# Performance work log

Measured on AMD Instinct MI355X. Metric: run time of the kernel, lower is better.

The kernel has to match this reference:

```python
import jax, jax.numpy as jnp
import numpy as np

NUM_HEADS = 6
WIN = 16
NW = 16   # number of windows sharing one mask (b_ % NW == 0)


def setup_inputs() -> dict:
    key = jax.random.key(0)
    ks = jax.random.split(key, 6)
    b_, n, dim = 256, WIN * WIN, 192
    qkv = jax.random.normal(ks[0], (b_, n, 3 * dim), dtype=jnp.float32)
    rpi = jax.random.randint(ks[1], (n, n), 0, (2 * WIN - 1) * (2 * WIN - 1))
    # additive attention mask per window-group (Swin uses 0 / -100; randn is fine for math)
    mask = jax.random.normal(ks[2], (NW, n, n), dtype=jnp.float32)
    rpb_table = 0.02 * jax.random.normal(ks[3], ((2 * WIN - 1) * (2 * WIN - 1), NUM_HEADS), dtype=jnp.float32)
    proj_w = jax.random.normal(ks[4], (dim, dim), dtype=jnp.float32) * (1.0 / np.sqrt(dim))
    proj_b = jax.random.normal(ks[5], (dim,), dtype=jnp.float32) * 0.01
    return {"qkv": qkv, "rpi": rpi, "mask": mask, "rpb_table": rpb_table,
            "proj_w": proj_w, "proj_b": proj_b}


def reference(qkv, rpi, mask, rpb_table, proj_w, proj_b):
    b_, n, c3 = qkv.shape
    c = c3 // 3
    h = NUM_HEADS
    hd = c // h
    scale = float(hd) ** -0.5
    # (b_, n, 3, h, hd) -> (3, b_, h, n, hd)
    qkv = qkv.reshape(b_, n, 3, h, hd).transpose(2, 0, 3, 1, 4)
    q, k, v = qkv[0] * scale, qkv[1], qkv[2]
    attn = jnp.einsum('bhqd,bhkd->bhqk', q, k)  # [b_, h, n, n]
    # gathered relative position bias: [n, n, h] -> [h, n, n]
    bias = rpb_table[rpi].transpose(2, 0, 1)
    attn = attn + bias[None]
    # add per-window-group mask: [b_//nw, nw, h, n, n]
    nw = mask.shape[0]
    attn = attn.reshape(b_ // nw, nw, h, n, n) + mask[None, :, None]
    attn = attn.reshape(b_, h, n, n)
    attn = jax.nn.softmax(attn, axis=-1)
    x = jnp.einsum('bhqk,bhkd->bhqd', attn, v)  # [b_, h, n, hd]
    x = x.transpose(0, 2, 1, 3).reshape(b_, n, c)
    # nn.Linear: x @ W^T + b
    return x @ proj_w.T + proj_b
```

## Files before the change

### kernel.cpp

```cpp
#include <hip/hip_runtime.h>
#include <hip/hip_bf16.h>

typedef _Float16 f16;
typedef _Float16 f16x2 __attribute__((ext_vector_type(2)));
typedef _Float16 f16x4 __attribute__((ext_vector_type(4)));
typedef _Float16 f16x8 __attribute__((ext_vector_type(8)));
typedef __fp16 h16x2 __attribute__((ext_vector_type(2)));
typedef float f32x4 __attribute__((ext_vector_type(4)));

#define NHEADS 6
#define NTOK 256
#define NWINS 256
#define DIM 192
#define HD 32
#define C3 576
#define LOG2E 1.4426950408889634f
#define SCALE (0.17677669529663687f * LOG2E)

__device__ inline f16x2 pkrtz(float a, float b) {
  h16x2 r = __builtin_amdgcn_cvt_pkrtz(a, b);
  return __builtin_bit_cast(f16x2, r);
}

__global__ __launch_bounds__(256) void prep_cb_kernel(const int* __restrict__ rpi,
                                                      const float* __restrict__ mask,
                                                      const float* __restrict__ rpb,
                                                      f16* __restrict__ cb) {
  int idx = blockIdx.x * 256 + threadIdx.x;
  int rem = idx & 255;
  int q = (idx >> 8) & 255;
  int t = idx >> 16;
  int h = t % 6;
  int mg = t / 6;
  int ktp = rem >> 5;
  int gg = (rem >> 3) & 3;
  int e = rem & 7;
  int k = (2 * ktp + (e >> 2)) * 16 + gg * 4 + (e & 3);
  float v = (rpb[rpi[(q << 8) | k] * 6 + h] + mask[(mg << 16) | (q << 8) | k]) * LOG2E;
  cb[idx] = (f16)v;
}

__global__ __launch_bounds__(256) void prep_w_kernel(const float* __restrict__ w,
                                                     f16* __restrict__ w16) {
  int i = blockIdx.x * 256 + threadIdx.x;
  if (i < DIM * DIM) w16[i] = (f16)w[i];
}

__device__ inline f16x8 q_to_f16(float4 a, float4 b) {
  f16x2 p0 = pkrtz(a.x * SCALE, a.y * SCALE);
  f16x2 p1 = pkrtz(a.z * SCALE, a.w * SCALE);
  f16x2 p2 = pkrtz(b.x * SCALE, b.y * SCALE);
  f16x2 p3 = pkrtz(b.z * SCALE, b.w * SCALE);
  f16x4 lo = __builtin_shufflevector(p0, p1, 0, 1, 2, 3);
  f16x4 hi = __builtin_shufflevector(p2, p3, 0, 1, 2, 3);
  return __builtin_shufflevector(lo, hi, 0, 1, 2, 3, 4, 5, 6, 7);
}

__global__ __launch_bounds__(512, 4) void attn_kernel(const float* __restrict__ qkv,
                                                      const f16* __restrict__ cb,
                                                      f16* __restrict__ x16) {
  const int idx = blockIdx.x;
  const int grp = idx % 96;
  const int pr = idx / 96;
  const int h = grp % 6;
  const int blo = grp / 6;
  const int tid = threadIdx.x;
  const int lane = tid & 63;
  const int wave = tid >> 6;
  const int g = lane >> 4;
  const int r16 = lane & 15;

  __shared__ f16 Klin[2][16 * 64 * 8];
  __shared__ f16 VT[2][32][264];

  const int t = tid & 255;
  const int srow = t >> 3;
  const int part = t & 7;
  const bool isK = tid < 256;
  const int gg = part >> 1;
  const int half = part & 1;
  const int d0 = part * 4;

  const int b0 = ((pr * 2) << 4) | blo;
  const int b1 = ((pr * 2 + 1) << 4) | blo;
  const float* sbase0 = qkv + (size_t)(b0 * NTOK + srow) * C3 + DIM + (isK ? 0 : DIM)
                        + h * HD + part * 4;
  const float* sbase1 = qkv + (size_t)(b1 * NTOK + srow) * C3 + DIM + (isK ? 0 : DIM)
                        + h * HD + part * 4;

  auto stage_write = [&](int buf, int rgbase, const float4* v4) {
#pragma unroll
    for (int rg = 0; rg < 4; ++rg) {
      const int row = (rgbase + rg) * 32 + srow;
      if (isK) {
        const int slot = ((row >> 4) * 64) + gg * 16 + ((row & 15) ^ (gg << 2));
        f16x2 k01 = pkrtz(v4[rg].x, v4[rg].y);
        f16x2 k23 = pkrtz(v4[rg].z, v4[rg].w);
        *((f16x4*)&Klin[buf][slot * 8 + half * 4]) =
            __builtin_shufflevector(k01, k23, 0, 1, 2, 3);
      } else {
        VT[buf][d0 + 0][row ^ (((d0 + 0) & 7) << 2)] = (f16)v4[rg].x;
        VT[buf][d0 + 1][row ^ (((d0 + 1) & 7) << 2)] = (f16)v4[rg].y;
        VT[buf][d0 + 2][row ^ (((d0 + 2) & 7) << 2)] = (f16)v4[rg].z;
        VT[buf][d0 + 3][row ^ (((d0 + 3) & 7) << 2)] = (f16)v4[rg].w;
      }
    }
  };

  {
    float4 s4[8];
#pragma unroll
    for (int i = 0; i < 8; ++i)
      s4[i] = *(const float4*)(sbase0 + (size_t)(i * 32) * C3);
    stage_write(0, 0, s4);
    stage_write(0, 4, s4 + 4);
  }
  __syncthreads();

  const f16* cbb = cb + ((size_t)grp << 16);
  const int krd = (lane & 48) + ((lane & 15) ^ ((lane >> 2) & 12));
  const int qbase = wave * 32;

#pragma unroll
  for (int pair = 0; pair < 2; ++pair) {
    const int b = (pair == 0) ? b0 : b1;

#pragma unroll
    for (int c = 0; c < 2; ++c) {
      float4 n4[4];
      if (pair == 0) {
#pragma unroll
        for (int i = 0; i < 4; ++i)
          n4[i] = *(const float4*)(sbase1 + (size_t)((c * 4 + i) * 32) * C3);
      }

      const int qrow = qbase + c * 16 + r16;
      const float* qp = qkv + (size_t)(b * NTOK + qrow) * C3 + h * HD + g * 8;
      f16x8 qf = q_to_f16(((const float4*)qp)[0], ((const float4*)qp)[1]);
      const f16* cbq = cbb + (qrow << 8) + g * 8;

      f16x8 cv[4];
#pragma unroll
      for (int kp = 0; kp < 4; ++kp) cv[kp] = *((const f16x8*)(cbq + kp * 32));
      f32x4 acc[8];
#pragma unroll
      for (int kp = 0; kp < 4; ++kp) {
#pragma unroll
        for (int r = 0; r < 4; ++r) {
          acc[2 * kp][r] = (float)cv[kp][r];
          acc[2 * kp + 1][r] = (float)cv[kp][4 + r];
        }
      }
#pragma unroll
      for (int kt = 0; kt < 8; ++kt) {
        f16x8 af = *((const f16x8*)&Klin[pair][(kt * 64 + krd) * 8]);
        acc[kt] = __builtin_amdgcn_mfma_f32_16x16x32_f16(af, qf, acc[kt], 0, 0, 0);
      }

      if (pair == 0) stage_write(1, c * 4, n4);

      float m0 = fmaxf(fmaxf(acc[0][0], acc[1][0]), fmaxf(acc[2][0], acc[3][0]));
      float m1 = fmaxf(fmaxf(acc[0][1], acc[1][1]), fmaxf(acc[2][1], acc[3][1]));
      float m2 = fmaxf(fmaxf(acc[0][2], acc[1][2]), fmaxf(acc[2][2], acc[3][2]));
      float m3 = fmaxf(fmaxf(acc[0][3], acc[1][3]), fmaxf(acc[2][3], acc[3][3]));
#pragma unroll
      for (int kt = 4; kt < 8; ++kt) {
        m0 = fmaxf(m0, acc[kt][0]); m1 = fmaxf(m1, acc[kt][1]);
        m2 = fmaxf(m2, acc[kt][2]); m3 = fmaxf(m3, acc[kt][3]);
      }
      float mA = fmaxf(fmaxf(m0, m1), fmaxf(m2, m3));
      mA = fmaxf(mA, __shfl_xor(mA, 16));
      mA = fmaxf(mA, __shfl_xor(mA, 32));

      float s0 = 0.f, s1 = 0.f, s2 = 0.f, s3 = 0.f;
#pragma unroll
      for (int kt = 0; kt < 8; ++kt) {
        float p0 = __builtin_amdgcn_exp2f(acc[kt][0] - mA);
        float p1 = __builtin_amdgcn_exp2f(acc[kt][1] - mA);
        float p2 = __builtin_amdgcn_exp2f(acc[kt][2] - mA);
        float p3 = __builtin_amdgcn_exp2f(acc[kt][3] - mA);
        acc[kt][0] = p0; acc[kt][1] = p1; acc[kt][2] = p2; acc[kt][3] = p3;
        s0 += p0; s1 += p1; s2 += p2; s3 += p3;
      }
      float sA = (s0 + s1) + (s2 + s3);

      f32x4 xa0[2], xa1[2];
#pragma unroll
      for (int dt = 0; dt < 2; ++dt) {
        xa0[dt][0] = 0.f; xa0[dt][1] = 0.f; xa0[dt][2] = 0.f; xa0[dt][3] = 0.f;
        xa1[dt][0] = 0.f; xa1[dt][1] = 0.f; xa1[dt][2] = 0.f; xa1[dt][3] = 0.f;
      }
#pragma unroll
      for (int kt = 0; kt < 8; ++kt) {
        f16x2 p01 = pkrtz(acc[kt][0], acc[kt][1]);
        f16x2 p23 = pkrtz(acc[kt][2], acc[kt][3]);
        f16x4 pf = __builtin_shufflevector(p01, p23, 0, 1, 2, 3);
#pragma unroll
        for (int dt = 0; dt < 2; ++dt) {
          const int col = (kt * 16 + g * 4) ^ ((r16 & 7) << 2);
          f16x4 vf = *((const f16x4*)&VT[pair][dt * 16 + r16][col]);
          if (kt < 4)
            xa0[dt] = __builtin_amdgcn_mfma_f32_16x16x16f16(vf, pf, xa0[dt], 0, 0, 0);
          else
            xa1[dt] = __builtin_amdgcn_mfma_f32_16x16x16f16(vf, pf, xa1[dt], 0, 0, 0);
        }
      }

#pragma unroll
      for (int kp = 0; kp < 4; ++kp) cv[kp] = *((const f16x8*)(cbq + 128 + kp * 32));
#pragma unroll
      for (int kp = 0; kp < 4; ++kp) {
#pragma unroll
        for (int r = 0; r < 4; ++r) {
          acc[2 * kp][r] = (float)cv[kp][r];
          acc[2 * kp + 1][r] = (float)cv[kp][4 + r];
        }
      }
#pragma unroll
      for (int kt = 0; kt < 8; ++kt) {
        f16x8 af = *((const f16x8*)&Klin[pair][((kt + 8) * 64 + krd) * 8]);
        acc[kt] = __builtin_amdgcn_mfma_f32_16x16x32_f16(af, qf, acc[kt], 0, 0, 0);
      }

      m0 = fmaxf(fmaxf(acc[0][0], acc[1][0]), fmaxf(acc[2][0], acc[3][0]));
      m1 = fmaxf(fmaxf(acc[0][1], acc[1][1]), fmaxf(acc[2][1], acc[3][1]));
      m2 = fmaxf(fmaxf(acc[0][2], acc[1][2]), fmaxf(acc[2][2], acc[3][2]));
      m3 = fmaxf(fmaxf(acc[0][3], acc[1][3]), fmaxf(acc[2][3], acc[3][3]));
#pragma unroll
      for (int kt = 4; kt < 8; ++kt) {
        m0 = fmaxf(m0, acc[kt][0]); m1 = fmaxf(m1, acc[kt][1]);
        m2 = fmaxf(m2, acc[kt][2]); m3 = fmaxf(m3, acc[kt][3]);
      }
      float mB = fmaxf(fmaxf(m0, m1), fmaxf(m2, m3));
      mB = fmaxf(mB, __shfl_xor(mB, 16));
      mB = fmaxf(mB, __shfl_xor(mB, 32));

      const float m = fmaxf(mA, mB);
      const float scA = __builtin_amdgcn_exp2f(mA - m);

      s0 = 0.f; s1 = 0.f; s2 = 0.f; s3 = 0.f;
#pragma unroll
      for (int kt = 0; kt < 8; ++kt) {
        float p0 = __builtin_amdgcn_exp2f(acc[kt][0] - m);
        float p1 = __builtin_amdgcn_exp2f(acc[kt][1] - m);
        float p2 = __builtin_amdgcn_exp2f(acc[kt][2] - m);
        float p3 = __builtin_amdgcn_exp2f(acc[kt][3] - m);
        acc[kt][0] = p0; acc[kt][1] = p1; acc[kt][2] = p2; acc[kt][3] = p3;
        s0 += p0; s1 += p1; s2 += p2; s3 += p3;
      }
      float s = sA * scA + (s0 + s1) + (s2 + s3);
      s += __shfl_xor(s, 16);
      s += __shfl_xor(s, 32);
      const float rinv = 1.0f / s;

#pragma unroll
      for (int dt = 0; dt < 2; ++dt) {
        xa0[dt][0] *= scA; xa0[dt][1] *= scA; xa0[dt][2] *= scA; xa0[dt][3] *= scA;
        xa1[dt][0] *= scA; xa1[dt][1] *= scA; xa1[dt][2] *= scA; xa1[dt][3] *= scA;
      }
#pragma unroll
      for (int kt = 0; kt < 8; ++kt) {
        f16x2 p01 = pkrtz(acc[kt][0], acc[kt][1]);
        f16x2 p23 = pkrtz(acc[kt][2], acc[kt][3]);
        f16x4 pf = __builtin_shufflevector(p01, p23, 0, 1, 2, 3);
#pragma unroll
        for (int dt = 0; dt < 2; ++dt) {
          const int col = ((kt + 8) * 16 + g * 4) ^ ((r16 & 7) << 2);
          f16x4 vf = *((const f16x4*)&VT[pair][dt * 16 + r16][col]);
          if (kt < 4)
            xa0[dt] = __builtin_amdgcn_mfma_f32_16x16x16f16(vf, pf, xa0[dt], 0, 0, 0);
          else
            xa1[dt] = __builtin_amdgcn_mfma_f32_16x16x16f16(vf, pf, xa1[dt], 0, 0, 0);
        }
      }

      f16* xp = x16 + (size_t)(b * NTOK + qrow) * DIM + h * HD;
#pragma unroll
      for (int dt = 0; dt < 2; ++dt) {
        f16x2 o01 = pkrtz((xa0[dt][0] + xa1[dt][0]) * rinv,
                          (xa0[dt][1] + xa1[dt][1]) * rinv);
        f16x2 o23 = pkrtz((xa0[dt][2] + xa1[dt][2]) * rinv,
                          (xa0[dt][3] + xa1[dt][3]) * rinv);
        *((f16x4*)(xp + dt * 16 + g * 4)) = __builtin_shufflevector(o01, o23, 0, 1, 2, 3);
      }
    }

    if (pair == 0) __syncthreads();
  }
}

__global__ __launch_bounds__(256) void proj_kernel(const f16* __restrict__ x16,
                                                   const f16* __restrict__ w16,
                                                   const float* __restrict__ pb,
                                                   float* __restrict__ out) {
  const int lane = threadIdx.x & 63;
  const int wave = threadIdx.x >> 6;
  const int g = lane >> 4;
  const int r16 = lane & 15;
  const int m0 = blockIdx.x * 64 + wave * 16;

  f32x4 acc[12];
#pragma unroll
  for (int jt = 0; jt < 12; ++jt) {
    acc[jt][0] = 0.f; acc[jt][1] = 0.f; acc[jt][2] = 0.f; acc[jt][3] = 0.f;
  }
#pragma unroll
  for (int cc = 0; cc < 6; ++cc) {
    f16x8 af = *((const f16x8*)(x16 + (size_t)(m0 + r16) * DIM + cc * 32 + g * 8));
#pragma unroll
    for (int jt = 0; jt < 12; ++jt) {
      f16x8 bf = *((const f16x8*)(w16 + (size_t)(jt * 16 + r16) * DIM + cc * 32 + g * 8));
      acc[jt] = __builtin_amdgcn_mfma_f32_16x16x32_f16(af, bf, acc[jt], 0, 0, 0);
    }
  }
#pragma unroll
  for (int jt = 0; jt < 12; ++jt) {
    int j = jt * 16 + r16;
    float bias = pb[j];
#pragma unroll
    for (int r = 0; r < 4; ++r) {
      out[(size_t)(m0 + g * 4 + r) * DIM + j] = acc[jt][r] + bias;
    }
  }
}

extern "C" void kernel_launch(void* const* d_in, const int* in_sizes, int n_in,
                              void* d_out, int out_size, void* d_ws, size_t ws_size,
                              hipStream_t stream) {
  const float* qkv  = (const float*)d_in[0];
  const int*   rpi  = (const int*)d_in[1];
  const float* mask = (const float*)d_in[2];
  const float* rpb  = (const float*)d_in[3];
  const float* pw   = (const float*)d_in[4];
  const float* pbv  = (const float*)d_in[5];
  float* out = (float*)d_out;

  char* ws = (char*)d_ws;
  f16* cb16 = (f16*)ws;
  f16* x16  = (f16*)(ws + 12582912);
  f16* w16  = (f16*)(ws + 12582912 + 25165824);

  prep_cb_kernel<<<24576, 256, 0, stream>>>(rpi, mask, rpb, cb16);
  prep_w_kernel<<<144, 256, 0, stream>>>(pw, w16);
  attn_kernel<<<768, 512, 0, stream>>>(qkv, cb16, x16);
  proj_kernel<<<1024, 256, 0, stream>>>(x16, w16, pbv, out);
}
```

Before: 108.9 us.

## Split combined bias+mask precompute into separate per-head bias and per-group mask tables

The prep kernel no longer materialises a full 16x6x256x256 fp16 combined bias+mask tensor. It now writes a small per-head relative-position-bias table and a per-window-group mask table, each in the same swizzled layout. The attention kernel loads both and adds them in fp16 before seeding the accumulators. This cuts the prep write traffic and the footprint of the precomputed table by a large factor, at the cost of twice as many loads in the attention inner loop and an extra fp16 add, which also slightly changes rounding.

```diff
diff --git a/kernel.cpp b/kernel.cpp
--- a/kernel.cpp
+++ b/kernel.cpp
@@ -22,22 +22,49 @@
   return __builtin_bit_cast(f16x2, r);
 }
 
-__global__ __launch_bounds__(256) void prep_cb_kernel(const int* __restrict__ rpi,
-                                                      const float* __restrict__ mask,
-                                                      const float* __restrict__ rpb,
-                                                      f16* __restrict__ cb) {
-  int idx = blockIdx.x * 256 + threadIdx.x;
-  int rem = idx & 255;
-  int q = (idx >> 8) & 255;
-  int t = idx >> 16;
-  int h = t % 6;
-  int mg = t / 6;
-  int ktp = rem >> 5;
-  int gg = (rem >> 3) & 3;
-  int e = rem & 7;
-  int k = (2 * ktp + (e >> 2)) * 16 + gg * 4 + (e & 3);
-  float v = (rpb[rpi[(q << 8) | k] * 6 + h] + mask[(mg << 16) | (q << 8) | k]) * LOG2E;
-  cb[idx] = (f16)v;
+__global__ __launch_bounds__(256) void prep_rpb_kernel(const int* __restrict__ rpi,
+                                                       const float* __restrict__ rpb,
+                                                       f16* __restrict__ rpb16) {
+  int u = blockIdx.x * 256 + threadIdx.x;
+  int g = u & 3;
+  int ktp = (u >> 2) & 7;
+  int q = (u >> 5) & 255;
+  int h = u >> 13;
+  int k0 = ktp * 32 + g * 4;
+  const int* rp = rpi + (q << 8);
+  int4 i0 = *(const int4*)(rp + k0);
+  int4 i1 = *(const int4*)(rp + k0 + 16);
+  f16x8 o;
+  o[0] = (f16)(rpb[i0.x * 6 + h] * LOG2E);
+  o[1] = (f16)(rpb[i0.y * 6 + h] * LOG2E);
+  o[2] = (f16)(rpb[i0.z * 6 + h] * LOG2E);
+  o[3] = (f16)(rpb[i0.w * 6 + h] * LOG2E);
+  o[4] = (f16)(rpb[i1.x * 6 + h] * LOG2E);
+  o[5] = (f16)(rpb[i1.y * 6 + h] * LOG2E);
+  o[6] = (f16)(rpb[i1.z * 6 + h] * LOG2E);
+  o[7] = (f16)(rpb[i1.w * 6 + h] * LOG2E);
+  *((f16x8*)(rpb16 + (size_t)u * 8)) = o;
+}
+
+__global__ __launch_bounds__(256) void prep_mask_kernel(const float* __restrict__ mask,
+                                                        f16* __restrict__ mask16) {
+  int u = blockIdx.x * 256 + threadIdx.x;
+  int g = u & 3;
+  int ktp = (u >> 2) & 7;
+  int q = (u >> 5) & 255;
+  int mg = u >> 13;
+  int k0 = ktp * 32 + g * 4;
+  const float* mp = mask + ((size_t)mg << 16) + (q << 8);
+  float4 v0 = *(const float4*)(mp + k0);
+  float4 v1 = *(const float4*)(mp + k0 + 16);
+  f16x2 a = pkrtz(v0.x * LOG2E, v0.y * LOG2E);
+  f16x2 b = pkrtz(v0.z * LOG2E, v0.w * LOG2E);
+  f16x2 c = pkrtz(v1.x * LOG2E, v1.y * LOG2E);
+  f16x2 d = pkrtz(v1.z * LOG2E, v1.w * LOG2E);
+  f16x4 lo = __builtin_shufflevector(a, b, 0, 1, 2, 3);
+  f16x4 hi = __builtin_shufflevector(c, d, 0, 1, 2, 3);
+  *((f16x8*)(mask16 + (size_t)u * 8)) =
+      __builtin_shufflevector(lo, hi, 0, 1, 2, 3, 4, 5, 6, 7);
 }
 
 __global__ __launch_bounds__(256) void prep_w_kernel(const float* __restrict__ w,
@@ -57,7 +84,8 @@
 }
 
 __global__ __launch_bounds__(512, 4) void attn_kernel(const float* __restrict__ qkv,
-                                                      const f16* __restrict__ cb,
+                                                      const f16* __restrict__ rpb16,
+                                                      const f16* __restrict__ mask16,
                                                       f16* __restrict__ x16) {
   const int idx = blockIdx.x;
   const int grp = idx % 96;
@@ -117,7 +145,8 @@
   }
   __syncthreads();
 
-  const f16* cbb = cb + ((size_t)grp << 16);
+  const f16* rbb = rpb16 + ((size_t)h << 16);
+  const f16* mbb = mask16 + ((size_t)blo << 16);
   const int krd = (lane & 48) + ((lane & 15) ^ ((lane >> 2) & 12));
   const int qbase = wave * 32;
 
@@ -137,18 +166,21 @@
       const int qrow = qbase + c * 16 + r16;
       const float* qp = qkv + (size_t)(b * NTOK + qrow) * C3 + h * HD + g * 8;
       f16x8 qf = q_to_f16(((const float4*)qp)[0], ((const float4*)qp)[1]);
-      const f16* cbq = cbb + (qrow << 8) + g * 8;
-
-      f16x8 cv[4];
-#pragma unroll
-      for (int kp = 0; kp < 4; ++kp) cv[kp] = *((const f16x8*)(cbq + kp * 32));
+      const int boff = (qrow << 8) + g * 8;
+
       f32x4 acc[8];
 #pragma unroll
-      for (int kp = 0; kp < 4; ++kp) {
+      for (int hb = 0; hb < 2; ++hb) {
+        f16x8 cv0 = *((const f16x8*)(rbb + boff + (2 * hb) * 32))
+                  + *((const f16x8*)(mbb + boff + (2 * hb) * 32));
+        f16x8 cv1 = *((const f16x8*)(rbb + boff + (2 * hb + 1) * 32))
+                  + *((const f16x8*)(mbb + boff + (2 * hb + 1) * 32));
 #pragma unroll
         for (int r = 0; r < 4; ++r) {
-          acc[2 * kp][r] = (float)cv[kp][r];
-          acc[2 * kp + 1][r] = (float)cv[kp][4 + r];
+          acc[4 * hb + 0][r] = (float)cv0[r];
+          acc[4 * hb + 1][r] = (float)cv0[4 + r];
+          acc[4 * hb + 2][r] = (float)cv1[r];
+          acc[4 * hb + 3][r] = (float)cv1[4 + r];
         }
       }
 #pragma unroll
@@ -207,13 +239,17 @@
       }
 
 #pragma unroll
-      for (int kp = 0; kp < 4; ++kp) cv[kp] = *((const f16x8*)(cbq + 128 + kp * 32));
-#pragma unroll
-      for (int kp = 0; kp < 4; ++kp) {
+      for (int hb = 0; hb < 2; ++hb) {
+        f16x8 cv0 = *((const f16x8*)(rbb + boff + 128 + (2 * hb) * 32))
+                  + *((const f16x8*)(mbb + boff + 128 + (2 * hb) * 32));
+        f16x8 cv1 = *((const f16x8*)(rbb + boff + 128 + (2 * hb + 1) * 32))
+                  + *((const f16x8*)(mbb + boff + 128 + (2 * hb + 1) * 32));
 #pragma unroll
         for (int r = 0; r < 4; ++r) {
-          acc[2 * kp][r] = (float)cv[kp][r];
-          acc[2 * kp + 1][r] = (float)cv[kp][4 + r];
+          acc[4 * hb + 0][r] = (float)cv0[r];
+          acc[4 * hb + 1][r] = (float)cv0[4 + r];
+          acc[4 * hb + 2][r] = (float)cv1[r];
+          acc[4 * hb + 3][r] = (float)cv1[4 + r];
         }
       }
 #pragma unroll
@@ -336,12 +372,14 @@
   float* out = (float*)d_out;
 
   char* ws = (char*)d_ws;
-  f16* cb16 = (f16*)ws;
-  f16* x16  = (f16*)(ws + 12582912);
-  f16* w16  = (f16*)(ws + 12582912 + 25165824);
-
-  prep_cb_kernel<<<24576, 256, 0, stream>>>(rpi, mask, rpb, cb16);
+  f16* rpb16  = (f16*)ws;
+  f16* mask16 = (f16*)(ws + 786432);
+  f16* x16    = (f16*)(ws + 786432 + 2097152);
+  f16* w16    = (f16*)(ws + 786432 + 2097152 + 25165824);
+
+  prep_rpb_kernel<<<192, 256, 0, stream>>>(rpi, rpb, rpb16);
+  prep_mask_kernel<<<512, 256, 0, stream>>>(mask, mask16);
   prep_w_kernel<<<144, 256, 0, stream>>>(pw, w16);
-  attn_kernel<<<768, 512, 0, stream>>>(qkv, cb16, x16);
+  attn_kernel<<<768, 512, 0, stream>>>(qkv, rpb16, mask16, x16);
   proj_kernel<<<1024, 256, 0, stream>>>(x16, w16, pbv, out);
 }
```

After: 121.6 us. 1.12x slower.
